# Performance work log

Hardware: AMD Instinct MI355X
Metric: run time of the kernel (lower is better)

The kernel has to match this reference:

```python
import jax, jax.numpy as jnp
import numpy as np

LN_EPS = 1e-5
BN_EPS = 1e-5
ATTN_EPS = 1e-6

def _ln(x, g, b):
    m = x.mean(-1, keepdims=True)
    v = x.var(-1, keepdims=True)
    return (x - m) / jnp.sqrt(v + LN_EPS) * g + b

def setup_inputs() -> dict:
    key = jax.random.key(0)
    ks = jax.random.split(key, 16)
    B, C, N = 4, 256, 8192
    s = 0.05
    def rn(k, shape, scale=1.0):
        return jax.random.normal(k, shape, jnp.float32) * scale
    return {
        "x1": rn(ks[0], (B, C, N)),
        "x2": rn(ks[1], (B, C, N)),
        "Wq": rn(ks[2], (C, C), s), "bq": rn(ks[3], (C,), s),
        "Wk": rn(ks[4], (C, C), s), "bk": rn(ks[5], (C,), s),
        "Wv": rn(ks[6], (C, C), s), "bv": rn(ks[7], (C,), s),
        "threshold": jnp.array([0.1], jnp.float32),
        "W1": rn(ks[8], (2 * C, 2 * C), s),
        "W2": rn(ks[9], (C, 2 * C), s),
        "g1": jnp.ones((C,), jnp.float32), "b1": jnp.zeros((C,), jnp.float32),
        "g2": jnp.ones((C,), jnp.float32), "b2": jnp.zeros((C,), jnp.float32),
        "Wa": rn(ks[10], (C, C), s), "ba": rn(ks[11], (C,), s),
        "bn_g": jnp.ones((C,), jnp.float32), "bn_b": jnp.zeros((C,), jnp.float32),
        "bn_m": jnp.zeros((C,), jnp.float32), "bn_v": jnp.ones((C,), jnp.float32),
    }

def reference(x1, x2, Wq, bq, Wk, bk, Wv, bv, threshold, W1, W2,
              g1, b1, g2, b2, Wa, ba, bn_g, bn_b, bn_m, bn_v):
    B, C, N = x1.shape
    H = 4
    d = C // H
    def conv1x1(x, W, b):  # nn.Conv1d(C, C, 1): [B,C,N] -> [B,C,N]
        return jnp.einsum('bcn,oc->bon', x, W) + b[:, None]
    # projections -> [B, N, H, d]
    q = conv1x1(x1, Wq, bq).transpose(0, 2, 1).reshape(B, N, H, d)
    k = conv1x1(x2, Wk, bk).transpose(0, 2, 1).reshape(B, N, H, d)
    v = conv1x1(x2, Wv, bv).transpose(0, 2, 1).reshape(B, N, H, d)
    # DynamicSparseLinearAttention
    Q = jax.nn.elu(q) + 1.0
    K = jax.nn.elu(k) + 1.0
    S = v.shape[1]
    vals = v / S
    KV = jnp.einsum('nshd,nshv->nhdv', K, vals)               # [B,H,d,d]
    scores = jnp.einsum('nlhd,nhd->nlh', Q, K.sum(axis=1))    # [B,N,H]
    sparse = jnp.where(scores > threshold[0], scores, 0.0)
    Z = 1.0 / (sparse + ATTN_EPS)
    msg = jnp.einsum('nlhd,nhdv,nlh->nlhv', Q, KV, Z) * S     # [B,N,H,d]
    # view [B,N,C]; the transpose(1,2).transpose(1,2) in torch cancels
    msg = msg.reshape(B, N, H * d)
    msg = _ln(msg, g1, b1)
    msg = jnp.concatenate([x1.transpose(0, 2, 1), msg], axis=2)  # [B,N,2C]
    msg = jax.nn.relu(msg @ W1.T) @ W2.T                         # [B,N,C]
    msg = _ln(msg, g2, b2).transpose(0, 2, 1)                    # [B,C,N]
    # aug shortcut: conv1x1 + BatchNorm1d (eval mode, running stats)
    aug = conv1x1(x1, Wa, ba)
    aug = (aug - bn_m[None, :, None]) / jnp.sqrt(bn_v[None, :, None] + BN_EPS)
    aug = aug * bn_g[None, :, None] + bn_b[None, :, None]
    return msg + x1 + aug
```

## Files before the change

### kernel.cpp

```cpp
#include <hip/hip_runtime.h>

#define BB 4
#define CC 256
#define NN 8192
#define HH 4
#define NCH 16

typedef unsigned short u16;
typedef __bf16 bf16x8 __attribute__((ext_vector_type(8)));
typedef float f32x4 __attribute__((ext_vector_type(4)));

__device__ __forceinline__ float bf2f(unsigned u) {
  return __uint_as_float(u << 16);
}
__device__ __forceinline__ u16 f2bf(float f) {
  unsigned u = __float_as_uint(f);
  return (u16)((u + 0x7fffu + ((u >> 16) & 1u)) >> 16);
}
__device__ __forceinline__ void bf8_to_f32(uint4 r, float* f) {
  f[0] = __uint_as_float(r.x << 16); f[1] = __uint_as_float(r.x & 0xffff0000u);
  f[2] = __uint_as_float(r.y << 16); f[3] = __uint_as_float(r.y & 0xffff0000u);
  f[4] = __uint_as_float(r.z << 16); f[5] = __uint_as_float(r.z & 0xffff0000u);
  f[6] = __uint_as_float(r.w << 16); f[7] = __uint_as_float(r.w & 0xffff0000u);
}
__device__ __forceinline__ void gload16(const u16* g, u16* l) {
  __builtin_amdgcn_global_load_lds(
      (const __attribute__((address_space(1))) unsigned int*)g,
      (__attribute__((address_space(3))) unsigned int*)l, 16, 0, 0);
}

__global__ __launch_bounds__(256) void cvt_all_kernel(
    const float* __restrict__ wq, const float* __restrict__ wk,
    const float* __restrict__ wv, const float* __restrict__ wa,
    const float* __restrict__ w1, const float* __restrict__ w2,
    u16* __restrict__ oq, u16* __restrict__ ok, u16* __restrict__ ov,
    u16* __restrict__ oa, u16* __restrict__ o1, u16* __restrict__ o2) {
  int i = blockIdx.x * 256 + threadIdx.x;
  const float* src;
  u16* dst;
  int off;
  if (i < 65536) { src = wq; dst = oq; off = i; }
  else if (i < 131072) { src = wk; dst = ok; off = i - 65536; }
  else if (i < 196608) { src = wv; dst = ov; off = i - 131072; }
  else if (i < 262144) { src = wa; dst = oa; off = i - 196608; }
  else if (i < 524288) { src = w1; dst = o1; off = i - 262144; }
  else { src = w2; dst = o2; off = i - 524288; }
  dst[off] = f2bf(src[off]);
}

__global__ __launch_bounds__(256) void transpose_kernel(const float* __restrict__ x1,
                                                        const float* __restrict__ x2,
                                                        u16* __restrict__ x1t,
                                                        u16* __restrict__ x2t) {
  __shared__ float T[64][65];
  const int bz = blockIdx.z;
  const int b = bz & 3;
  const float* x = (bz < 4) ? x1 : x2;
  u16* xt = (bz < 4) ? x1t : x2t;
  const int c0 = blockIdx.y * 64, n0 = blockIdx.x * 64;
  const float* xp = x + ((size_t)b * CC + c0) * NN + n0;
#pragma unroll
  for (int it = 0; it < 4; ++it) {
    int idx = threadIdx.x + it * 256;
    int r = idx >> 4, seg = idx & 15;
    float4 v = *(const float4*)(xp + (size_t)r * NN + seg * 4);
    T[r][seg * 4 + 0] = v.x; T[r][seg * 4 + 1] = v.y;
    T[r][seg * 4 + 2] = v.z; T[r][seg * 4 + 3] = v.w;
  }
  __syncthreads();
  u16* op = xt + ((size_t)b * NN + n0) * CC + c0;
  const int j = threadIdx.x >> 2, g = threadIdx.x & 3;
#pragma unroll
  for (int i = 0; i < 4; ++i) {
    int c = g * 16 + i * 4;
    uint2 pk;
    pk.x = (unsigned)f2bf(T[c + 0][j]) | ((unsigned)f2bf(T[c + 1][j]) << 16);
    pk.y = (unsigned)f2bf(T[c + 2][j]) | ((unsigned)f2bf(T[c + 3][j]) << 16);
    *(uint2*)(op + (size_t)j * CC + c) = pk;
  }
}

__global__ __launch_bounds__(256) void proj_all_kernel(
    const u16* __restrict__ x1t, const u16* __restrict__ x2t,
    const u16* __restrict__ Wqb, const u16* __restrict__ Wkb,
    const u16* __restrict__ Wvb, const u16* __restrict__ Wab,
    const float* __restrict__ bq, const float* __restrict__ bk,
    const float* __restrict__ bv, const float* __restrict__ ba,
    const float* __restrict__ bng, const float* __restrict__ bnb,
    const float* __restrict__ bnm, const float* __restrict__ bnv,
    u16* __restrict__ Qt, u16* __restrict__ K2, u16* __restrict__ V2,
    u16* __restrict__ augt) {
  __shared__ u16 lds[2 * 128 * 72];
  u16* As = lds;
  u16* Ws = lds + 128 * 72;
  u16* T = lds;
  const int mode = blockIdx.z;
  const u16* A = (mode == 0 || mode == 3) ? x1t : x2t;
  const u16* W = (mode == 0) ? Wqb : (mode == 1) ? Wkb : (mode == 2) ? Wvb : Wab;
  const float* bias = (mode == 0) ? bq : (mode == 1) ? bk : (mode == 2) ? bv : ba;
  u16* outp = (mode == 0) ? Qt : (mode == 1) ? K2 : (mode == 2) ? V2 : augt;
  const int m0 = blockIdx.x * 128, o0 = blockIdx.y * 128;
  const int tid = threadIdx.x, lane = tid & 63, wave = tid >> 6;
  const int wm = (wave >> 1) * 64, wo = (wave & 1) * 64;
  const int fr = lane & 15, fq = lane >> 4;
  f32x4 acc[4][4] = {};
  for (int kt = 0; kt < 4; ++kt) {
    const int k0 = kt << 6;
#pragma unroll
    for (int i = 0; i < 4; ++i) {
      int idx = tid + i * 256;
      int r = idx >> 3, s = idx & 7;
      *(uint4*)(&As[r * 72 + s * 8]) = *(const uint4*)(A + (size_t)(m0 + r) * CC + k0 + s * 8);
      *(uint4*)(&Ws[r * 72 + s * 8]) = *(const uint4*)(W + (size_t)(o0 + r) * CC + k0 + s * 8);
    }
    __syncthreads();
#pragma unroll
    for (int kk = 0; kk < 2; ++kk) {
      bf16x8 af[4], bfr[4];
#pragma unroll
      for (int mi = 0; mi < 4; ++mi)
        af[mi] = __builtin_bit_cast(bf16x8, *(const uint4*)(&As[(wm + mi * 16 + fr) * 72 + kk * 32 + fq * 8]));
#pragma unroll
      for (int oi = 0; oi < 4; ++oi)
        bfr[oi] = __builtin_bit_cast(bf16x8, *(const uint4*)(&Ws[(wo + oi * 16 + fr) * 72 + kk * 32 + fq * 8]));
#pragma unroll
      for (int mi = 0; mi < 4; ++mi)
#pragma unroll
        for (int oi = 0; oi < 4; ++oi)
          acc[mi][oi] = __builtin_amdgcn_mfma_f32_16x16x32_bf16(af[mi], bfr[oi], acc[mi][oi], 0, 0, 0);
    }
    __syncthreads();
  }
  const int bb_ = m0 >> 13;
  const int nb = m0 & (NN - 1);
#pragma unroll
  for (int oi = 0; oi < 4; ++oi) {
    const int o_loc = wo + oi * 16 + fr;
    const int col = o0 + o_loc;
    float b0 = bias[col], sc = 1.f, sh = 0.f;
    if (mode == 3) {
      sc = bng[col] * rsqrtf(bnv[col] + 1e-5f);
      sh = (b0 - bnm[col]) * sc + bnb[col];
    }
#pragma unroll
    for (int mi = 0; mi < 4; ++mi) {
      const int mbase = wm + mi * 16 + fq * 4;
      float v[4];
#pragma unroll
      for (int r = 0; r < 4; ++r) {
        float t = acc[mi][oi][r];
        if (mode == 0 || mode == 1) {
          t += b0;
          t = (t > 0.f) ? (t + 1.f) : __expf(t);
        } else if (mode == 2) {
          t += b0;
        } else {
          t = t * sc + sh;
        }
        v[r] = t;
      }
      if (mode == 1 || mode == 2) {
#pragma unroll
        for (int e = 0; e < 2; ++e) {
          unsigned pk = (unsigned)f2bf(v[2 * e]) | ((unsigned)f2bf(v[2 * e + 1]) << 16);
          *(unsigned*)(&T[o_loc * 132 + mbase + 2 * e]) = pk;
        }
      } else {
#pragma unroll
        for (int r = 0; r < 4; ++r) T[(mbase + r) * 132 + o_loc] = f2bf(v[r]);
      }
    }
  }
  __syncthreads();
#pragma unroll
  for (int i = 0; i < 8; ++i) {
    int idx = tid + i * 256;
    int r = idx >> 4, c = (idx & 15) * 8;
    uint4 d = *(const uint4*)(&T[r * 132 + c]);
    if (mode == 1 || mode == 2) {
      *(uint4*)(outp + ((size_t)bb_ * CC + o0 + r) * NN + nb + c) = d;
    } else {
      *(uint4*)(outp + (size_t)(m0 + r) * CC + o0 + c) = d;
    }
  }
}

__global__ __launch_bounds__(256) void kvpartial_kernel(const u16* __restrict__ K2,
                                                        const u16* __restrict__ V2,
                                                        float* __restrict__ Pkv,
                                                        float* __restrict__ Pks) {
  __shared__ u16 Ks[64 * 64];
  __shared__ u16 Vs[64 * 64];
  const int b = blockIdx.z, h = blockIdx.y, ch = blockIdx.x;
  const int tid = threadIdx.x, lane = tid & 63, w = tid >> 6;
  const int fr = lane & 15, fq = lane >> 4;
  const size_t base = ((size_t)b * CC + h * 64) * NN + (size_t)ch * (NN / NCH);
  f32x4 acc[4] = {};
  const int krow = tid >> 2, kq = tid & 3;
  float ksacc = 0.f;
  for (int step = 0; step < (NN / NCH) / 64; ++step) {
#pragma unroll
    for (int i = 0; i < 2; ++i) {
      int idx = tid + i * 256;
      int rr = idx >> 3, ss = idx & 7;
      gload16(K2 + base + (size_t)rr * NN + step * 64 + ss * 8, &Ks[(i * 256 + w * 64) * 8]);
      gload16(V2 + base + (size_t)rr * NN + step * 64 + ss * 8, &Vs[(i * 256 + w * 64) * 8]);
    }
    __syncthreads();
#pragma unroll
    for (int j = 0; j < 16; ++j) ksacc += bf2f(Ks[krow * 64 + kq * 16 + j]);
#pragma unroll
    for (int kk = 0; kk < 2; ++kk) {
      bf16x8 af = __builtin_bit_cast(bf16x8, *(const uint4*)(&Ks[(w * 16 + fr) * 64 + kk * 32 + fq * 8]));
#pragma unroll
      for (int oi = 0; oi < 4; ++oi) {
        bf16x8 bfr = __builtin_bit_cast(bf16x8, *(const uint4*)(&Vs[(oi * 16 + fr) * 64 + kk * 32 + fq * 8]));
        acc[oi] = __builtin_amdgcn_mfma_f32_16x16x32_bf16(af, bfr, acc[oi], 0, 0, 0);
      }
    }
    __syncthreads();
  }
  ksacc += __shfl_xor(ksacc, 1);
  ksacc += __shfl_xor(ksacc, 2);
  if (kq == 0) Pks[((size_t)ch * BB + b) * CC + h * 64 + krow] = ksacc;
  float* o = Pkv + (((size_t)ch * (BB * HH) + b * HH + h) << 12);
#pragma unroll
  for (int oi = 0; oi < 4; ++oi)
#pragma unroll
    for (int r = 0; r < 4; ++r)
      o[(w * 16 + fq * 4 + r) * 64 + oi * 16 + fr] = acc[oi][r];
}

__global__ __launch_bounds__(256) void kvreduce_kernel(const float* __restrict__ Pkv,
                                                       const float* __restrict__ Pks,
                                                       u16* __restrict__ KVT,
                                                       float* __restrict__ Ksum) {
  int i = blockIdx.x * 256 + threadIdx.x;
  int bh = i >> 12, dk = (i >> 6) & 63, dv = i & 63;
  float s = 0.f;
#pragma unroll
  for (int ch = 0; ch < NCH; ++ch)
    s += Pkv[(((size_t)ch * (BB * HH) + bh) << 12) + (dk << 6) + dv];
  KVT[((size_t)bh << 12) + (dv << 6) + dk] = f2bf(s);
  if (i < BB * CC) {
    float t = 0.f;
#pragma unroll
    for (int ch = 0; ch < NCH; ++ch) t += Pks[ch * (BB * CC) + i];
    Ksum[i] = t;
  }
}

__global__ __launch_bounds__(256) void bigmsg_kernel(const u16* __restrict__ Qt,
                                                     const u16* __restrict__ KVT,
                                                     const float* __restrict__ Ksum,
                                                     const float* __restrict__ thrp,
                                                     const float* __restrict__ g1,
                                                     const float* __restrict__ b1,
                                                     u16* __restrict__ msgN) {
  __shared__ u16 lds[64 * 264 + 4 * 64 * 72];
  __shared__ float Zs[64 * 4];
  u16* As = lds;
  u16* Ws = lds + 64 * 264;
  u16* Ml = lds;
  const int m0 = blockIdx.x * 64;
  const int b = blockIdx.z;
  const int tid = threadIdx.x, lane = tid & 63, w = tid >> 6;
  const int fr = lane & 15, fq = lane >> 4;
  const u16* Ap = Qt + ((size_t)b * NN + m0) * CC;
#pragma unroll
  for (int i = 0; i < 8; ++i) {
    int idx = tid + i * 256;
    int rr = idx >> 5, ss = idx & 31;
    *(uint4*)(&As[rr * 264 + ss * 8]) = *(const uint4*)(Ap + (size_t)rr * CC + ss * 8);
  }
  const u16* Wp = KVT + ((size_t)(b * HH) << 12);
#pragma unroll
  for (int i = 0; i < 8; ++i) {
    int idx = tid + i * 256;
    int h = idx >> 9, rr = (idx >> 3) & 63, ss = idx & 7;
    *(uint4*)(&Ws[(h * 64 + rr) * 72 + ss * 8]) = *(const uint4*)(Wp + ((size_t)h << 12) + rr * 64 + ss * 8);
  }
  __syncthreads();
  {
    const int row = tid >> 2, h = tid & 3;
    const float* ks = Ksum + b * CC + h * 64;
    float za = 0.f;
#pragma unroll
    for (int j8 = 0; j8 < 8; ++j8) {
      uint4 raw = *(const uint4*)(&As[row * 264 + h * 64 + j8 * 8]);
      float f[8];
      bf8_to_f32(raw, f);
#pragma unroll
      for (int j = 0; j < 8; ++j) za += f[j] * ks[j8 * 8 + j];
    }
    const float thrv = thrp[0];
    Zs[row * 4 + h] = 1.f / (((za > thrv) ? za : 0.f) + 1e-6f);
  }
  f32x4 acc[4][4] = {};
#pragma unroll
  for (int kk = 0; kk < 2; ++kk) {
    bf16x8 af[4], bfr[4];
#pragma unroll
    for (int mi = 0; mi < 4; ++mi)
      af[mi] = __builtin_bit_cast(bf16x8, *(const uint4*)(&As[(mi * 16 + fr) * 264 + w * 64 + kk * 32 + fq * 8]));
#pragma unroll
    for (int oi = 0; oi < 4; ++oi)
      bfr[oi] = __builtin_bit_cast(bf16x8, *(const uint4*)(&Ws[(w * 64 + oi * 16 + fr) * 72 + kk * 32 + fq * 8]));
#pragma unroll
    for (int mi = 0; mi < 4; ++mi)
#pragma unroll
      for (int oi = 0; oi < 4; ++oi)
        acc[mi][oi] = __builtin_amdgcn_mfma_f32_16x16x32_bf16(af[mi], bfr[oi], acc[mi][oi], 0, 0, 0);
  }
  __syncthreads();
#pragma unroll
  for (int oi = 0; oi < 4; ++oi) {
    const int col = w * 64 + oi * 16 + fr;
#pragma unroll
    for (int mi = 0; mi < 4; ++mi) {
#pragma unroll
      for (int r = 0; r < 4; ++r) {
        const int row = mi * 16 + fq * 4 + r;
        Ml[row * 272 + col] = f2bf(acc[mi][oi][r] * Zs[row * 4 + w]);
      }
    }
  }
  __syncthreads();
  {
    const int row = tid >> 2, q = tid & 3;
    const u16* mrow = &Ml[row * 272 + q * 64];
    float s1 = 0.f, s2 = 0.f;
#pragma unroll
    for (int j8 = 0; j8 < 8; ++j8) {
      uint4 raw = *(const uint4*)(mrow + j8 * 8);
      float f[8];
      bf8_to_f32(raw, f);
#pragma unroll
      for (int j = 0; j < 8; ++j) {
        s1 += f[j];
        s2 += f[j] * f[j];
      }
    }
    s1 += __shfl_xor(s1, 1); s2 += __shfl_xor(s2, 1);
    s1 += __shfl_xor(s1, 2); s2 += __shfl_xor(s2, 2);
    const float mean = s1 * (1.f / CC);
    const float var = s2 * (1.f / CC) - mean * mean;
    const float rs = rsqrtf(var + 1e-5f);
    u16* orow = msgN + ((size_t)b * NN + m0 + row) * CC + q * 64;
#pragma unroll
    for (int j8 = 0; j8 < 8; ++j8) {
      uint4 raw = *(const uint4*)(mrow + j8 * 8);
      float f[8];
      bf8_to_f32(raw, f);
      const int cb = q * 64 + j8 * 8;
      unsigned pk[4];
#pragma unroll
      for (int e = 0; e < 4; ++e) {
        float lo = (f[2 * e] - mean) * rs * g1[cb + 2 * e] + b1[cb + 2 * e];
        float hi = (f[2 * e + 1] - mean) * rs * g1[cb + 2 * e + 1] + b1[cb + 2 * e + 1];
        pk[e] = (unsigned)f2bf(lo) | ((unsigned)f2bf(hi) << 16);
      }
      *(uint4*)(orow + j8 * 8) = make_uint4(pk[0], pk[1], pk[2], pk[3]);
    }
  }
}

__global__ __launch_bounds__(256) void mlp1_kernel(const u16* __restrict__ A1,
                                                   const u16* __restrict__ A2,
                                                   const u16* __restrict__ W,
                                                   u16* __restrict__ outp) {
  __shared__ u16 lds[2 * 128 * 72];
  u16* As = lds;
  u16* Ws = lds + 128 * 72;
  u16* T = lds;
  const int m0 = blockIdx.x * 128, o0 = blockIdx.y * 128;
  const int tid = threadIdx.x, lane = tid & 63, wave = tid >> 6;
  const int wm = (wave >> 1) * 64, wo = (wave & 1) * 64;
  const int fr = lane & 15, fq = lane >> 4;
  f32x4 acc[4][4] = {};
  for (int kt = 0; kt < 8; ++kt) {
    const int k0 = kt << 6;
    const u16* Ap = (k0 < 256) ? (A1 + k0) : (A2 + (k0 - 256));
#pragma unroll
    for (int i = 0; i < 4; ++i) {
      int idx = tid + i * 256;
      int r = idx >> 3, s = idx & 7;
      *(uint4*)(&As[r * 72 + s * 8]) = *(const uint4*)(Ap + (size_t)(m0 + r) * CC + s * 8);
      *(uint4*)(&Ws[r * 72 + s * 8]) = *(const uint4*)(W + (size_t)(o0 + r) * 512 + k0 + s * 8);
    }
    __syncthreads();
#pragma unroll
    for (int kk = 0; kk < 2; ++kk) {
      bf16x8 af[4], bfr[4];
#pragma unroll
      for (int mi = 0; mi < 4; ++mi)
        af[mi] = __builtin_bit_cast(bf16x8, *(const uint4*)(&As[(wm + mi * 16 + fr) * 72 + kk * 32 + fq * 8]));
#pragma unroll
      for (int oi = 0; oi < 4; ++oi)
        bfr[oi] = __builtin_bit_cast(bf16x8, *(const uint4*)(&Ws[(wo + oi * 16 + fr) * 72 + kk * 32 + fq * 8]));
#pragma unroll
      for (int mi = 0; mi < 4; ++mi)
#pragma unroll
        for (int oi = 0; oi < 4; ++oi)
          acc[mi][oi] = __builtin_amdgcn_mfma_f32_16x16x32_bf16(af[mi], bfr[oi], acc[mi][oi], 0, 0, 0);
    }
    __syncthreads();
  }
#pragma unroll
  for (int oi = 0; oi < 4; ++oi) {
    const int o_loc = wo + oi * 16 + fr;
#pragma unroll
    for (int mi = 0; mi < 4; ++mi) {
      const int mbase = wm + mi * 16 + fq * 4;
#pragma unroll
      for (int r = 0; r < 4; ++r)
        T[(mbase + r) * 132 + o_loc] = f2bf(fmaxf(acc[mi][oi][r], 0.f));
    }
  }
  __syncthreads();
#pragma unroll
  for (int i = 0; i < 8; ++i) {
    int idx = tid + i * 256;
    int r = idx >> 4, c = (idx & 15) * 8;
    *(uint4*)(outp + (size_t)(m0 + r) * 512 + o0 + c) = *(const uint4*)(&T[r * 132 + c]);
  }
}

__global__ __launch_bounds__(512) void mlp2fused_kernel(const u16* __restrict__ h1,
                                                        const u16* __restrict__ W2b,
                                                        const u16* __restrict__ augt,
                                                        const float* __restrict__ x1,
                                                        const float* __restrict__ g2,
                                                        const float* __restrict__ b2,
                                                        float* __restrict__ outp) {
  __shared__ u16 lds[128 * 272];
  u16* As = lds;
  u16* Ws = lds + 128 * 72;
  u16* Tl = lds;
  const int m0 = blockIdx.x * 128;
  const int b = m0 >> 13, nb = m0 & (NN - 1);
  const int tid = threadIdx.x, lane = tid & 63, w = tid >> 6;
  const int wm = (w >> 2) * 64, wo = (w & 3) * 64;
  const int fr = lane & 15, fq = lane >> 4;
  f32x4 acc[4][4] = {};
  for (int kt = 0; kt < 8; ++kt) {
    const int k0 = kt << 6;
#pragma unroll
    for (int i = 0; i < 2; ++i) {
      int idx = tid + i * 512;
      int rr = idx >> 3, ss = idx & 7;
      *(uint4*)(&As[rr * 72 + ss * 8]) = *(const uint4*)(h1 + (size_t)(m0 + rr) * 512 + k0 + ss * 8);
    }
#pragma unroll
    for (int i = 0; i < 4; ++i) {
      int idx = tid + i * 512;
      int rr = idx >> 3, ss = idx & 7;
      *(uint4*)(&Ws[rr * 72 + ss * 8]) = *(const uint4*)(W2b + (size_t)rr * 512 + k0 + ss * 8);
    }
    __syncthreads();
#pragma unroll
    for (int kk = 0; kk < 2; ++kk) {
      bf16x8 af[4], bfr[4];
#pragma unroll
      for (int mi = 0; mi < 4; ++mi)
        af[mi] = __builtin_bit_cast(bf16x8, *(const uint4*)(&As[(wm + mi * 16 + fr) * 72 + kk * 32 + fq * 8]));
#pragma unroll
      for (int oi = 0; oi < 4; ++oi)
        bfr[oi] = __builtin_bit_cast(bf16x8, *(const uint4*)(&Ws[(wo + oi * 16 + fr) * 72 + kk * 32 + fq * 8]));
#pragma unroll
      for (int mi = 0; mi < 4; ++mi)
#pragma unroll
        for (int oi = 0; oi < 4; ++oi)
          acc[mi][oi] = __builtin_amdgcn_mfma_f32_16x16x32_bf16(af[mi], bfr[oi], acc[mi][oi], 0, 0, 0);
    }
    __syncthreads();
  }
#pragma unroll
  for (int oi = 0; oi < 4; ++oi) {
    const int col = wo + oi * 16 + fr;
#pragma unroll
    for (int mi = 0; mi < 4; ++mi) {
#pragma unroll
      for (int r = 0; r < 4; ++r) {
        const int row = wm + mi * 16 + fq * 4 + r;
        Tl[row * 272 + col] = f2bf(acc[mi][oi][r]);
      }
    }
  }
  __syncthreads();
  {
    const int row = tid >> 2, q = tid & 3;
    u16* mrow = &Tl[row * 272 + q * 64];
    float s1 = 0.f, s2 = 0.f;
#pragma unroll
    for (int j8 = 0; j8 < 8; ++j8) {
      uint4 raw = *(const uint4*)(mrow + j8 * 8);
      float f[8];
      bf8_to_f32(raw, f);
#pragma unroll
      for (int j = 0; j < 8; ++j) {
        s1 += f[j];
        s2 += f[j] * f[j];
      }
    }
    s1 += __shfl_xor(s1, 1); s2 += __shfl_xor(s2, 1);
    s1 += __shfl_xor(s1, 2); s2 += __shfl_xor(s2, 2);
    const float mean = s1 * (1.f / CC);
    const float var = s2 * (1.f / CC) - mean * mean;
    const float rs = rsqrtf(var + 1e-5f);
    const u16* arow = augt + ((size_t)b * NN + nb + row) * CC + q * 64;
#pragma unroll
    for (int j8 = 0; j8 < 8; ++j8) {
      uint4 raw = *(const uint4*)(mrow + j8 * 8);
      uint4 ar = *(const uint4*)(arow + j8 * 8);
      float f[8], af[8];
      bf8_to_f32(raw, f);
      bf8_to_f32(ar, af);
      const int cb = q * 64 + j8 * 8;
      unsigned pk[4];
#pragma unroll
      for (int e = 0; e < 4; ++e) {
        float lo = (f[2 * e] - mean) * rs * g2[cb + 2 * e] + b2[cb + 2 * e] + af[2 * e];
        float hi = (f[2 * e + 1] - mean) * rs * g2[cb + 2 * e + 1] + b2[cb + 2 * e + 1] + af[2 * e + 1];
        pk[e] = (unsigned)f2bf(lo) | ((unsigned)f2bf(hi) << 16);
      }
      *(uint4*)(mrow + j8 * 8) = make_uint4(pk[0], pk[1], pk[2], pk[3]);
    }
  }
  __syncthreads();
#pragma unroll
  for (int i = 0; i < 64; ++i) {
    int idx = tid + i * 512;
    int n = idx & 127, c = idx >> 7;
    size_t off = ((size_t)b * CC + c) * NN + nb + n;
    outp[off] = bf2f(Tl[n * 272 + c]) + x1[off];
  }
}

extern "C" void kernel_launch(void* const* d_in, const int* in_sizes, int n_in,
                              void* d_out, int out_size, void* d_ws, size_t ws_size,
                              hipStream_t stream) {
  (void)in_sizes; (void)n_in; (void)out_size; (void)ws_size;
  const float* x1 = (const float*)d_in[0];
  const float* x2 = (const float*)d_in[1];
  const float* Wq = (const float*)d_in[2];
  const float* bq = (const float*)d_in[3];
  const float* Wk = (const float*)d_in[4];
  const float* bk = (const float*)d_in[5];
  const float* Wv = (const float*)d_in[6];
  const float* bv = (const float*)d_in[7];
  const float* thr = (const float*)d_in[8];
  const float* W1 = (const float*)d_in[9];
  const float* W2 = (const float*)d_in[10];
  const float* g1 = (const float*)d_in[11];
  const float* b1 = (const float*)d_in[12];
  const float* g2 = (const float*)d_in[13];
  const float* b2 = (const float*)d_in[14];
  const float* Wa = (const float*)d_in[15];
  const float* ba = (const float*)d_in[16];
  const float* bng = (const float*)d_in[17];
  const float* bnb = (const float*)d_in[18];
  const float* bnm = (const float*)d_in[19];
  const float* bnv = (const float*)d_in[20];
  float* out = (float*)d_out;

  char* ws = (char*)d_ws;
  constexpr size_t SZ = (size_t)BB * NN * CC * sizeof(u16);
  u16* x1t = (u16*)(ws);
  u16* x2t = (u16*)(ws + SZ);
  u16* Qt = (u16*)(ws + 2 * SZ);
  u16* K2 = (u16*)(ws + 3 * SZ);
  u16* V2 = (u16*)(ws + 4 * SZ);
  u16* augt = (u16*)(ws + 5 * SZ);
  float* Pkv = (float*)(ws + 6 * SZ);
  u16* h1 = Qt;
  u16* msgN = V2;
  char* tail = ws + 7 * SZ;
  float* Ksum = (float*)tail;
  u16* KVT = (u16*)(tail + 4096);
  float* Pks = (float*)(tail + 4096 + 131072);
  u16* Wqb = (u16*)(tail + 4096 + 131072 + 65536);
  u16* Wkb = Wqb + CC * CC;
  u16* Wvb = Wkb + CC * CC;
  u16* Wab = Wvb + CC * CC;
  u16* W1b = Wab + CC * CC;
  u16* W2b = W1b + 512 * 512;

  cvt_all_kernel<<<dim3(2560), 256, 0, stream>>>(Wq, Wk, Wv, Wa, W1, W2,
                                                 Wqb, Wkb, Wvb, Wab, W1b, W2b);
  transpose_kernel<<<dim3(NN / 64, CC / 64, 2 * BB), 256, 0, stream>>>(x1, x2, x1t, x2t);
  proj_all_kernel<<<dim3(256, 2, 4), 256, 0, stream>>>(
      x1t, x2t, Wqb, Wkb, Wvb, Wab, bq, bk, bv, ba, bng, bnb, bnm, bnv,
      Qt, K2, V2, augt);
  kvpartial_kernel<<<dim3(NCH, HH, BB), 256, 0, stream>>>(K2, V2, Pkv, Pks);
  kvreduce_kernel<<<dim3(256), 256, 0, stream>>>(Pkv, Pks, KVT, Ksum);
  bigmsg_kernel<<<dim3(NN / 64, 1, BB), 256, 0, stream>>>(Qt, KVT, Ksum, thr, g1, b1, msgN);
  mlp1_kernel<<<dim3(256, 4), 256, 0, stream>>>(x1t, msgN, W1b, h1);
  mlp2fused_kernel<<<dim3(256), 512, 0, stream>>>(h1, W2b, augt, x1, g2, b2, out);
}
```

Before: 179.9 us.

## Split fused MLP2+LayerNorm kernel into separate GEMM and LN/transpose kernels

```diff
diff --git a/kernel.cpp b/kernel.cpp
--- a/kernel.cpp
+++ b/kernel.cpp
@@ -426,36 +426,26 @@
   }
 }
 
-__global__ __launch_bounds__(512) void mlp2fused_kernel(const u16* __restrict__ h1,
-                                                        const u16* __restrict__ W2b,
-                                                        const u16* __restrict__ augt,
-                                                        const float* __restrict__ x1,
-                                                        const float* __restrict__ g2,
-                                                        const float* __restrict__ b2,
-                                                        float* __restrict__ outp) {
-  __shared__ u16 lds[128 * 272];
+__global__ __launch_bounds__(256) void mlp2_kernel(const u16* __restrict__ h1,
+                                                   const u16* __restrict__ W,
+                                                   u16* __restrict__ outp) {
+  __shared__ u16 lds[2 * 128 * 72];
   u16* As = lds;
   u16* Ws = lds + 128 * 72;
-  u16* Tl = lds;
-  const int m0 = blockIdx.x * 128;
-  const int b = m0 >> 13, nb = m0 & (NN - 1);
-  const int tid = threadIdx.x, lane = tid & 63, w = tid >> 6;
-  const int wm = (w >> 2) * 64, wo = (w & 3) * 64;
+  u16* T = lds;
+  const int m0 = blockIdx.x * 128, o0 = blockIdx.y * 128;
+  const int tid = threadIdx.x, lane = tid & 63, wave = tid >> 6;
+  const int wm = (wave >> 1) * 64, wo = (wave & 1) * 64;
   const int fr = lane & 15, fq = lane >> 4;
   f32x4 acc[4][4] = {};
   for (int kt = 0; kt < 8; ++kt) {
     const int k0 = kt << 6;
 #pragma unroll
-    for (int i = 0; i < 2; ++i) {
-      int idx = tid + i * 512;
-      int rr = idx >> 3, ss = idx & 7;
-      *(uint4*)(&As[rr * 72 + ss * 8]) = *(const uint4*)(h1 + (size_t)(m0 + rr) * 512 + k0 + ss * 8);
-    }
-#pragma unroll
     for (int i = 0; i < 4; ++i) {
-      int idx = tid + i * 512;
-      int rr = idx >> 3, ss = idx & 7;
-      *(uint4*)(&Ws[rr * 72 + ss * 8]) = *(const uint4*)(W2b + (size_t)rr * 512 + k0 + ss * 8);
+      int idx = tid + i * 256;
+      int r = idx >> 3, s = idx & 7;
+      *(uint4*)(&As[r * 72 + s * 8]) = *(const uint4*)(h1 + (size_t)(m0 + r) * 512 + k0 + s * 8);
+      *(uint4*)(&Ws[r * 72 + s * 8]) = *(const uint4*)(W + (size_t)(o0 + r) * 512 + k0 + s * 8);
     }
     __syncthreads();
 #pragma unroll
@@ -477,26 +467,43 @@
   }
 #pragma unroll
   for (int oi = 0; oi < 4; ++oi) {
-    const int col = wo + oi * 16 + fr;
+    const int o_loc = wo + oi * 16 + fr;
 #pragma unroll
     for (int mi = 0; mi < 4; ++mi) {
-#pragma unroll
-      for (int r = 0; r < 4; ++r) {
-        const int row = wm + mi * 16 + fq * 4 + r;
-        Tl[row * 272 + col] = f2bf(acc[mi][oi][r]);
-      }
-    }
-  }
-  __syncthreads();
+      const int mbase = wm + mi * 16 + fq * 4;
+#pragma unroll
+      for (int r = 0; r < 4; ++r)
+        T[(mbase + r) * 132 + o_loc] = f2bf(acc[mi][oi][r]);
+    }
+  }
+  __syncthreads();
+#pragma unroll
+  for (int i = 0; i < 8; ++i) {
+    int idx = tid + i * 256;
+    int r = idx >> 4, c = (idx & 15) * 8;
+    *(uint4*)(outp + (size_t)(m0 + r) * CC + o0 + c) = *(const uint4*)(&T[r * 132 + c]);
+  }
+}
+
+__global__ __launch_bounds__(256) void lnaddT_kernel(const u16* __restrict__ mlp2b,
+                                                     const u16* __restrict__ augt,
+                                                     const float* __restrict__ x1,
+                                                     const float* __restrict__ g2,
+                                                     const float* __restrict__ b2,
+                                                     float* __restrict__ outp) {
+  __shared__ u16 T[256 * 67];
+  const int b = blockIdx.y, n0 = blockIdx.x * 64;
+  const int tid = threadIdx.x;
   {
-    const int row = tid >> 2, q = tid & 3;
-    u16* mrow = &Tl[row * 272 + q * 64];
+    const int r = tid >> 2, q = tid & 3;
+    const size_t rowoff = ((size_t)b * NN + n0 + r) * CC + q * 64;
+    uint4 raw[8];
     float s1 = 0.f, s2 = 0.f;
 #pragma unroll
     for (int j8 = 0; j8 < 8; ++j8) {
-      uint4 raw = *(const uint4*)(mrow + j8 * 8);
+      raw[j8] = *(const uint4*)(mlp2b + rowoff + j8 * 8);
       float f[8];
-      bf8_to_f32(raw, f);
+      bf8_to_f32(raw[j8], f);
 #pragma unroll
       for (int j = 0; j < 8; ++j) {
         s1 += f[j];
@@ -508,32 +515,27 @@
     const float mean = s1 * (1.f / CC);
     const float var = s2 * (1.f / CC) - mean * mean;
     const float rs = rsqrtf(var + 1e-5f);
-    const u16* arow = augt + ((size_t)b * NN + nb + row) * CC + q * 64;
 #pragma unroll
     for (int j8 = 0; j8 < 8; ++j8) {
-      uint4 raw = *(const uint4*)(mrow + j8 * 8);
-      uint4 ar = *(const uint4*)(arow + j8 * 8);
+      uint4 ar = *(const uint4*)(augt + rowoff + j8 * 8);
       float f[8], af[8];
-      bf8_to_f32(raw, f);
+      bf8_to_f32(raw[j8], f);
       bf8_to_f32(ar, af);
       const int cb = q * 64 + j8 * 8;
-      unsigned pk[4];
-#pragma unroll
-      for (int e = 0; e < 4; ++e) {
-        float lo = (f[2 * e] - mean) * rs * g2[cb + 2 * e] + b2[cb + 2 * e] + af[2 * e];
-        float hi = (f[2 * e + 1] - mean) * rs * g2[cb + 2 * e + 1] + b2[cb + 2 * e + 1] + af[2 * e + 1];
-        pk[e] = (unsigned)f2bf(lo) | ((unsigned)f2bf(hi) << 16);
-      }
-      *(uint4*)(mrow + j8 * 8) = make_uint4(pk[0], pk[1], pk[2], pk[3]);
+#pragma unroll
+      for (int e = 0; e < 8; ++e) {
+        float v = (f[e] - mean) * rs * g2[cb + e] + b2[cb + e] + af[e];
+        T[(cb + e) * 67 + r] = f2bf(v);
+      }
     }
   }
   __syncthreads();
 #pragma unroll
   for (int i = 0; i < 64; ++i) {
-    int idx = tid + i * 512;
-    int n = idx & 127, c = idx >> 7;
-    size_t off = ((size_t)b * CC + c) * NN + nb + n;
-    outp[off] = bf2f(Tl[n * 272 + c]) + x1[off];
+    int idx = tid + i * 256;
+    int c = idx >> 6, n = idx & 63;
+    size_t off = ((size_t)b * CC + c) * NN + n0 + n;
+    outp[off] = bf2f(T[c * 67 + n]) + x1[off];
   }
 }
 
@@ -575,6 +577,7 @@
   float* Pkv = (float*)(ws + 6 * SZ);
   u16* h1 = Qt;
   u16* msgN = V2;
+  u16* mlp2b = V2;
   char* tail = ws + 7 * SZ;
   float* Ksum = (float*)tail;
   u16* KVT = (u16*)(tail + 4096);
@@ -596,5 +599,6 @@
   kvreduce_kernel<<<dim3(256), 256, 0, stream>>>(Pkv, Pks, KVT, Ksum);
   bigmsg_kernel<<<dim3(NN / 64, 1, BB), 256, 0, stream>>>(Qt, KVT, Ksum, thr, g1, b1, msgN);
   mlp1_kernel<<<dim3(256, 4), 256, 0, stream>>>(x1t, msgN, W1b, h1);
-  mlp2fused_kernel<<<dim3(256), 512, 0, stream>>>(h1, W2b, augt, x1, g2, b2, out);
-}
+  mlp2_kernel<<<dim3(256, 2), 256, 0, stream>>>(h1, W2b, mlp2b);
+  lnaddT_kernel<<<dim3(NN / 64, BB), 256, 0, stream>>>(mlp2b, augt, x1, g2, b2, out);
+}
```

Measured after the change: 166.1 us. -7.7%, faster.
